# Kernel tuning notes

Hardware: AMD Instinct MI355X
Metric: run time of the kernel (lower is better)

The kernel has to match this reference:

```python
import jax, jax.numpy as jnp
import numpy as np

N_NODES = 10000
N_EDGES = 160000
IN_DIM, HID_DIM, OUT_DIM = 256, 512, 256


def gcn_conv(x, W, b, src, dst, dinv):
    # PyG GCNConv with add_self_loops=True and symmetric normalization.
    # dinv = deg^{-1/2} computed once (degrees include self loops).
    h = x @ W                                   # [N, F_out]
    norm = dinv[src] * dinv[dst]                # [E]
    msg = h[src] * norm[:, None]                # gather + scale, [E, F_out]
    agg = jnp.zeros_like(h).at[dst].add(msg)    # scatter-add over edges
    agg = agg + h * (dinv * dinv)[:, None]      # self-loop contribution
    return agg + b


def setup_inputs() -> dict:
    key = jax.random.key(0)
    ks = jax.random.split(key, 8)
    x = jax.random.normal(ks[0], (N_NODES, IN_DIM), dtype=jnp.float32)
    edge_index = jax.random.randint(ks[1], (2, N_EDGES), 0, N_NODES, dtype=jnp.int64)

    def glorot(k, fan_in, fan_out):
        s = jnp.sqrt(6.0 / (fan_in + fan_out)).astype(jnp.float32)
        return jax.random.uniform(k, (fan_in, fan_out), jnp.float32, -s, s)

    return {
        "x": x,
        "W1": glorot(ks[2], IN_DIM, HID_DIM), "b1": jnp.zeros((HID_DIM,), jnp.float32),
        "W2": glorot(ks[3], HID_DIM, HID_DIM), "b2": jnp.zeros((HID_DIM,), jnp.float32),
        "W3": glorot(ks[4], HID_DIM, OUT_DIM), "b3": jnp.zeros((OUT_DIM,), jnp.float32),
        "edge_index": edge_index,
    }


def reference(x, W1, b1, W2, b2, W3, b3, edge_index):
    src, dst = edge_index[0], edge_index[1]
    n = x.shape[0]
    # degree with self loops (edge weight 1), shared by all three layers
    deg = jnp.zeros((n,), x.dtype).at[dst].add(1.0) + 1.0
    dinv = jax.lax.rsqrt(deg)
    h = jnp.tanh(gcn_conv(x, W1, b1, src, dst, dinv))
    h = jnp.tanh(gcn_conv(h, W2, b2, src, dst, dinv))
    out = gcn_conv(h, W3, b3, src, dst, dinv)
    return out
```

## Files before the change

### kernel.cpp

```cpp
#include <hip/hip_runtime.h>
#include <math.h>

#define NN 10000
#define NE 160000
#define IN_DIM 256
#define HID_DIM 512
#define OUT_DIM 256

typedef unsigned short u16;
typedef _Float16 f16x8 __attribute__((ext_vector_type(8)));
typedef __attribute__((ext_vector_type(4))) float f32x4;


union F16U { _Float16 h; u16 u; };
static __device__ __forceinline__ u16 f2h_bits(float f) {
    F16U v; v.h = (_Float16)f; return v.u;
}

static __device__ __forceinline__ void gload_lds(const u16* g, uint4* l) {
    __builtin_amdgcn_global_load_lds((const __attribute__((address_space(1))) void*)g,
                                     (__attribute__((address_space(3))) void*)l,
                                     16, 0, 0);
}


__global__ void k_init(const float* __restrict__ W1, const float* __restrict__ W2,
                       const float* __restrict__ W3, const float* __restrict__ x,
                       u16* __restrict__ W1h, u16* __restrict__ W1l,
                       u16* __restrict__ W2h, u16* __restrict__ W2l,
                       u16* __restrict__ W3h, u16* __restrict__ W3l,
                       u16* __restrict__ xh, int* __restrict__ deg) {
    int idx = blockIdx.x * blockDim.x + threadIdx.x;
    const int S1 = IN_DIM * HID_DIM;
    const int S2 = HID_DIM * HID_DIM;
    const int S3 = HID_DIM * OUT_DIM;
    const int TW = S1 + S2 + S3;
    const int TX = NN * IN_DIM;
    if (idx < TW) {
        const float* W; u16 *Th, *Tl; int K, N, local;
        if (idx < S1)           { W = W1; Th = W1h; Tl = W1l; K = IN_DIM;  N = HID_DIM; local = idx; }
        else if (idx < S1 + S2) { W = W2; Th = W2h; Tl = W2l; K = HID_DIM; N = HID_DIM; local = idx - S1; }
        else                    { W = W3; Th = W3h; Tl = W3l; K = HID_DIM; N = OUT_DIM; local = idx - S1 - S2; }
        int k = local / N, n = local - k * N;
        float v = W[local];
        F16U hh; hh.h = (_Float16)v;
        float r = (v - (float)hh.h) * 2048.0f;
        Th[(size_t)n * K + k] = hh.u;
        Tl[(size_t)n * K + k] = f2h_bits(r);
    } else if (idx < TW + TX) {
        int j = idx - TW;
        xh[j] = f2h_bits(x[j]);
    } else if (idx < TW + TX + NN) {
        deg[idx - TW - TX] = 0;
    }
}


__global__ void k_count_deg(const int* __restrict__ dst, int* __restrict__ deg) {
    int e = blockIdx.x * blockDim.x + threadIdx.x;
    if (e < NE) atomicAdd(&deg[dst[e]], 1);
}

__launch_bounds__(1024)
__global__ void k_scan(const int* __restrict__ deg, int* __restrict__ row,
                       int* __restrict__ csr, float* __restrict__ dinv) {
    __shared__ int sdeg[10240];
    __shared__ int sums[1024];
    const int tid = threadIdx.x;
    for (int i = tid; i < NN; i += 1024) sdeg[i] = deg[i];
    __syncthreads();
    const int CH = 10;
    int base = tid * CH;
    int s = 0;
    for (int j = 0; j < CH; ++j) {
        int i = base + j;
        if (i < NN) s += sdeg[i] + 1;
    }
    sums[tid] = s;
    __syncthreads();
    for (int off = 1; off < 1024; off <<= 1) {
        int t = (tid >= off) ? sums[tid - off] : 0;
        __syncthreads();
        sums[tid] += t;
        __syncthreads();
    }
    int run = sums[tid] - s;
    for (int j = 0; j < CH; ++j) {
        int i = base + j;
        if (i < NN) {
            int dg = sdeg[i];
            csr[run] = i;
            row[i] = run + 1;
            dinv[i] = rsqrtf((float)dg + 1.0f);
            run += dg + 1;
        }
    }
}

__global__ void k_fill(const int* __restrict__ src, const int* __restrict__ dst,
                       int* __restrict__ row, int* __restrict__ csr) {
    int e = blockIdx.x * blockDim.x + threadIdx.x;
    if (e < NE) {
        int pos = atomicAdd(&row[dst[e]], 1);
        csr[pos] = src[e];
    }
}


template<int K, bool HAS_BIAS, bool DO_TANH, bool F16_OUT, bool ROWSCALE>
__launch_bounds__(256)
__global__ void k_gemm_f16x2(const u16* __restrict__ A, const u16* __restrict__ Bhi,
                             const u16* __restrict__ Blo,
                             const float* __restrict__ bias, const float* __restrict__ rowscale,
                             float* __restrict__ C, u16* __restrict__ Ch,
                             int M, int N, int MT, int MT8) {
    __shared__ uint4 As[2][512];
    __shared__ uint4 BsH[2][256];
    __shared__ uint4 BsL[2][256];

    const int id = blockIdx.x;
    const int xcd = id & 7;
    const int q2 = id >> 3;
    const int mt = (q2 % MT8) * 8 + xcd;
    const int nt = q2 / MT8;
    if (mt >= MT) return;

    const int tid  = threadIdx.x;
    const int wave = tid >> 6;
    const int lane = tid & 63;
    const int lr   = lane & 15;
    const int quad = lane >> 4;
    const int wm   = wave >> 1;
    const int wn   = wave & 1;
    const int m_base = mt * 128;
    const int n_base = nt * 64;

    const u16* gA  = A   + (size_t)(m_base + wave * 32 + lr) * K + quad * 8;
    const u16* gBh = Bhi + (size_t)(n_base + wave * 16 + lr) * K + quad * 8;
    const u16* gBl = Blo + (size_t)(n_base + wave * 16 + lr) * K + quad * 8;

    auto stage = [&](int buf, int it) {
        const int ko = it * 32;
        gload_lds(gA  + ko,          &As [buf][wave * 128]);
        gload_lds(gA  + ko + 16 * K, &As [buf][wave * 128 + 64]);
        gload_lds(gBh + ko,          &BsH[buf][wave * 64]);
        gload_lds(gBl + ko,          &BsL[buf][wave * 64]);
    };

    f32x4 accH[4][2] = {};
    f32x4 accL[4][2] = {};

    auto compute = [&](int buf) {
        f16x8 a[4], bH[2], bL[2];
#pragma unroll
        for (int tn = 0; tn < 2; ++tn) {
            int c = (wn * 2 + tn) * 64 + lane;
            bH[tn] = *(const f16x8*)&BsH[buf][c];
            bL[tn] = *(const f16x8*)&BsL[buf][c];
        }
#pragma unroll
        for (int tm = 0; tm < 4; ++tm)
            a[tm] = *(const f16x8*)&As[buf][(wm * 4 + tm) * 64 + lane];
#pragma unroll
        for (int tm = 0; tm < 4; ++tm)
#pragma unroll
            for (int tn = 0; tn < 2; ++tn) {
                accH[tm][tn] = __builtin_amdgcn_mfma_f32_16x16x32_f16(a[tm], bH[tn], accH[tm][tn], 0, 0, 0);
                accL[tm][tn] = __builtin_amdgcn_mfma_f32_16x16x32_f16(a[tm], bL[tn], accL[tm][tn], 0, 0, 0);
            }
    };

    const int NIT = K >> 5;

    stage(0, 0);
    __syncthreads();

    for (int it = 0; it < NIT; ++it) {
        if (it + 1 < NIT) stage((it + 1) & 1, it + 1);
        compute(it & 1);
        __syncthreads();
    }

#pragma unroll
    for (int tm = 0; tm < 4; ++tm) {
        int row0 = m_base + wm * 64 + tm * 16 + quad * 4;
#pragma unroll
        for (int i = 0; i < 4; ++i) {
            int row = row0 + i;
            if (row >= M) continue;
            float rs = ROWSCALE ? rowscale[row] : 1.0f;
#pragma unroll
            for (int tn = 0; tn < 2; ++tn) {
                int col = n_base + wn * 32 + tn * 16 + lr;
                float v = accH[tm][tn][i] + accL[tm][tn][i] * (1.0f / 2048.0f);
                if (HAS_BIAS) v += bias[col];
                if (DO_TANH) v = tanhf(v);
                if (ROWSCALE) v *= rs;
                if (F16_OUT) {
                    Ch[(size_t)row * N + col] = f2h_bits(v);
                } else {
                    C[(size_t)row * N + col] = v;
                }
            }
        }
    }
}


template<bool PRESCALED, bool HAS_BIAS, bool F16_OUT, int F>
__launch_bounds__(256)
__global__ void k_gather_h(const u16* __restrict__ h, const float* __restrict__ dinv,
                           const int* __restrict__ row_end, const int* __restrict__ csr,
                           const float* __restrict__ bias,
                           float* __restrict__ outF, u16* __restrict__ outH) {
    constexpr int L  = F / 8;
    constexpr int LS = L / 8;
    constexpr int NPB = 256 / LS;
    const int tid = threadIdx.x;
    const int d = (blockIdx.x >> 3) * NPB + tid / LS;
    if (d >= NN) return;
    const int f8 = (blockIdx.x & 7) * LS + (tid & (LS - 1));

    const int start = (d == 0) ? 0 : row_end[d - 1];
    const int end = row_end[d];
    const uint4* h16 = (const uint4*)h;

    float acc[8] = {};
    int e = start;
    for (; e + 8 <= end; e += 8) {
        int s[8]; uint4 raw[8]; float w[8];
#pragma unroll
        for (int j = 0; j < 8; ++j) s[j] = csr[e + j];
#pragma unroll
        for (int j = 0; j < 8; ++j) raw[j] = h16[(size_t)s[j] * L + f8];
#pragma unroll
        for (int j = 0; j < 8; ++j) w[j] = PRESCALED ? 1.0f : dinv[s[j]];
#pragma unroll
        for (int j = 0; j < 8; ++j) {
            f16x8 hv = *(const f16x8*)&raw[j];
#pragma unroll
            for (int t = 0; t < 8; ++t) acc[t] += w[j] * (float)hv[t];
        }
    }
    for (; e < end; ++e) {
        int s = csr[e];
        float w = PRESCALED ? 1.0f : dinv[s];
        uint4 raw = h16[(size_t)s * L + f8];
        f16x8 hv = *(const f16x8*)&raw;
#pragma unroll
        for (int t = 0; t < 8; ++t) acc[t] += w * (float)hv[t];
    }

    const float dd = dinv[d];
    float r[8];
#pragma unroll
    for (int t = 0; t < 8; ++t) r[t] = dd * acc[t];
    if (HAS_BIAS) {
        const float4* b4 = (const float4*)bias;
        float4 b0 = b4[f8 * 2], b1 = b4[f8 * 2 + 1];
        r[0] += b0.x; r[1] += b0.y; r[2] += b0.z; r[3] += b0.w;
        r[4] += b1.x; r[5] += b1.y; r[6] += b1.z; r[7] += b1.w;
    }
    if (F16_OUT) {
        union { u16 a[8]; uint4 v; } pk;
#pragma unroll
        for (int t = 0; t < 8; ++t) pk.a[t] = f2h_bits(r[t]);
        ((uint4*)outH)[(size_t)d * L + f8] = pk.v;
    } else {
        size_t base = (size_t)d * (F / 4) + f8 * 2;
        ((float4*)outF)[base]     = make_float4(r[0], r[1], r[2], r[3]);
        ((float4*)outF)[base + 1] = make_float4(r[4], r[5], r[6], r[7]);
    }
}


extern "C" void kernel_launch(void* const* d_in, const int* in_sizes, int n_in,
                              void* d_out, int out_size, void* d_ws, size_t ws_size,
                              hipStream_t stream) {
    const float* x  = (const float*)d_in[0];
    const float* W1 = (const float*)d_in[1];
    const float* b1 = (const float*)d_in[2];
    const float* W2 = (const float*)d_in[3];
    const float* b2 = (const float*)d_in[4];
    const float* W3 = (const float*)d_in[5];
    const float* b3 = (const float*)d_in[6];
    const int* edge = (const int*)d_in[7];
    const int* src = edge;
    const int* dst = edge + NE;
    float* out = (float*)d_out;

    const size_t SLOT = (size_t)NN * HID_DIM * 4;
    char* p = (char*)d_ws;
    char* slot0 = p;
    char* slot1 = p + SLOT;
    char* q = p + 2 * SLOT;
    u16* W1Th = (u16*)q; q += (size_t)IN_DIM  * HID_DIM * 2;
    u16* W1Tl = (u16*)q; q += (size_t)IN_DIM  * HID_DIM * 2;
    u16* W2Th = (u16*)q; q += (size_t)HID_DIM * HID_DIM * 2;
    u16* W2Tl = (u16*)q; q += (size_t)HID_DIM * HID_DIM * 2;
    u16* W3Th = (u16*)q; q += (size_t)HID_DIM * OUT_DIM * 2;
    u16* W3Tl = (u16*)q; q += (size_t)HID_DIM * OUT_DIM * 2;
    int*   deg  = (int*)q;   q += (size_t)NN * 4;
    float* dinv = (float*)q; q += (size_t)NN * 4;
    int*   row  = (int*)q;   q += (size_t)NN * 4;
    int*   csr  = (int*)q;   q += (size_t)(NE + NN) * 4;
    u16*   xh   = (u16*)q;   q += (size_t)NN * IN_DIM * 2;

    u16* Xagg  = (u16*)slot0;
    u16* g1h   = (u16*)slot1;
    u16* H1agg = (u16*)slot0;
    u16* h2    = (u16*)slot1;
    u16* g3h   = (u16*)slot0;

    const int T = 256;
    const int MT = (NN + 127) / 128;
    const int MT8 = (MT + 7) / 8;

    {
        int total = IN_DIM * HID_DIM + HID_DIM * HID_DIM + HID_DIM * OUT_DIM
                  + NN * IN_DIM + NN;
        k_init<<<(total + T - 1) / T, T, 0, stream>>>(W1, W2, W3, x, W1Th, W1Tl,
                                                      W2Th, W2Tl, W3Th, W3Tl, xh, deg);
    }
    k_count_deg<<<(NE + T - 1) / T, T, 0, stream>>>(dst, deg);
    k_scan<<<1, 1024, 0, stream>>>(deg, row, csr, dinv);
    k_fill<<<(NE + T - 1) / T, T, 0, stream>>>(src, dst, row, csr);

    const int G256 = ((NN + 63) / 64) * 8;
    const int G512 = ((NN + 31) / 32) * 8;
    const int GEMM_G512 = 8 * MT8 * (HID_DIM / 64);
    const int GEMM_G256 = 8 * MT8 * (OUT_DIM / 64);

    k_gather_h<false, false, true, IN_DIM><<<G256, 256, 0, stream>>>(
        xh, dinv, row, csr, nullptr, nullptr, Xagg);
    k_gemm_f16x2<IN_DIM, true, true, true, true><<<GEMM_G512, 256, 0, stream>>>(
        Xagg, W1Th, W1Tl, b1, dinv, nullptr, g1h, NN, HID_DIM, MT, MT8);

    k_gather_h<true, false, true, HID_DIM><<<G512, 256, 0, stream>>>(
        g1h, dinv, row, csr, nullptr, nullptr, H1agg);
    k_gemm_f16x2<HID_DIM, true, true, true, false><<<GEMM_G512, 256, 0, stream>>>(
        H1agg, W2Th, W2Tl, b2, nullptr, nullptr, h2, NN, HID_DIM, MT, MT8);

    k_gemm_f16x2<HID_DIM, false, false, true, true><<<GEMM_G256, 256, 0, stream>>>(
        h2, W3Th, W3Tl, nullptr, dinv, nullptr, g3h, NN, OUT_DIM, MT, MT8);
    k_gather_h<true, true, false, OUT_DIM><<<G256, 256, 0, stream>>>(
        g3h, dinv, row, csr, b3, out, nullptr);

    (void)in_sizes; (void)n_in; (void)out_size; (void)ws_size;
}
```

Measured before the change: 238.3 us.

## Fuse graph preprocessing kernels into one persistent kernel with grid barriers

Merges the init, degree count, scan and CSR fill kernels into a single persistent kernel of 512 blocks that uses atomic-counter grid barriers between phases, with a memset to zero the degree array and barrier counters. Weight and x conversion now runs after the CSR fill in the same kernel. The aim is to cut kernel launch overhead and the gaps between four small dependent launches. The risks are that a 512-block barrier needs every block co-resident to avoid deadlock, that the scan runs single-block while the other blocks spin, and that the grid-stride conversion loop serialises more work per thread.

Measured after the change: 671.0 us. +181.5%, slower.

```diff
diff --git a/kernel.cpp b/kernel.cpp
--- a/kernel.cpp
+++ b/kernel.cpp
@@ -7,6 +7,8 @@
 #define HID_DIM 512
 #define OUT_DIM 256
 
+#define PREP_GRID 512
+
 typedef unsigned short u16;
 typedef _Float16 f16x8 __attribute__((ext_vector_type(8)));
 typedef __attribute__((ext_vector_type(4))) float f32x4;
@@ -24,85 +26,93 @@
 }
 
 
-__global__ void k_init(const float* __restrict__ W1, const float* __restrict__ W2,
-                       const float* __restrict__ W3, const float* __restrict__ x,
-                       u16* __restrict__ W1h, u16* __restrict__ W1l,
-                       u16* __restrict__ W2h, u16* __restrict__ W2l,
-                       u16* __restrict__ W3h, u16* __restrict__ W3l,
-                       u16* __restrict__ xh, int* __restrict__ deg) {
-    int idx = blockIdx.x * blockDim.x + threadIdx.x;
+static __device__ __forceinline__ void gridbar(int* cnt) {
+    __syncthreads();
+    if (threadIdx.x == 0) {
+        __threadfence();
+        __hip_atomic_fetch_add(cnt, 1, __ATOMIC_ACQ_REL, __HIP_MEMORY_SCOPE_AGENT);
+        while (__hip_atomic_load(cnt, __ATOMIC_ACQUIRE, __HIP_MEMORY_SCOPE_AGENT) < PREP_GRID)
+            __builtin_amdgcn_s_sleep(1);
+    }
+    __syncthreads();
+}
+
+__global__ __launch_bounds__(256) void k_prep(
+    const float* __restrict__ W1, const float* __restrict__ W2,
+    const float* __restrict__ W3, const float* __restrict__ x,
+    const int* __restrict__ src, const int* __restrict__ dst,
+    u16* __restrict__ W1h, u16* __restrict__ W1l,
+    u16* __restrict__ W2h, u16* __restrict__ W2l,
+    u16* __restrict__ W3h, u16* __restrict__ W3l,
+    u16* __restrict__ xh, int* __restrict__ deg, int* __restrict__ row,
+    int* __restrict__ csr, float* __restrict__ dinv, int* __restrict__ bars) {
+    __shared__ int sdeg[10240];
+    __shared__ int psum[256];
+    const int tid = threadIdx.x;
+    const int gid = blockIdx.x * 256 + tid;
+    const int GS = PREP_GRID * 256;
+
+    for (int e = gid; e < NE; e += GS) atomicAdd(&deg[dst[e]], 1);
+    gridbar(&bars[0]);
+
+    if (blockIdx.x == 0) {
+        for (int i = tid; i < NN; i += 256)
+            sdeg[i] = __hip_atomic_load(&deg[i], __ATOMIC_RELAXED, __HIP_MEMORY_SCOPE_AGENT);
+        __syncthreads();
+        const int CH = 40;
+        const int base = tid * CH;
+        int s = 0;
+        for (int j = 0; j < CH; ++j) {
+            int i = base + j;
+            if (i < NN) s += sdeg[i] + 1;
+        }
+        psum[tid] = s;
+        __syncthreads();
+        for (int off = 1; off < 256; off <<= 1) {
+            int t = (tid >= off) ? psum[tid - off] : 0;
+            __syncthreads();
+            psum[tid] += t;
+            __syncthreads();
+        }
+        int run = psum[tid] - s;
+        for (int j = 0; j < CH; ++j) {
+            int i = base + j;
+            if (i < NN) {
+                int dg = sdeg[i];
+                csr[run] = i;
+                __hip_atomic_store(&row[i], run + 1, __ATOMIC_RELAXED, __HIP_MEMORY_SCOPE_AGENT);
+                dinv[i] = rsqrtf((float)dg + 1.0f);
+                run += dg + 1;
+            }
+        }
+    }
+    gridbar(&bars[1]);
+
+    for (int e = gid; e < NE; e += GS) {
+        int pos = atomicAdd(&row[dst[e]], 1);
+        csr[pos] = src[e];
+    }
     const int S1 = IN_DIM * HID_DIM;
     const int S2 = HID_DIM * HID_DIM;
     const int S3 = HID_DIM * OUT_DIM;
     const int TW = S1 + S2 + S3;
     const int TX = NN * IN_DIM;
-    if (idx < TW) {
-        const float* W; u16 *Th, *Tl; int K, N, local;
-        if (idx < S1)           { W = W1; Th = W1h; Tl = W1l; K = IN_DIM;  N = HID_DIM; local = idx; }
-        else if (idx < S1 + S2) { W = W2; Th = W2h; Tl = W2l; K = HID_DIM; N = HID_DIM; local = idx - S1; }
-        else                    { W = W3; Th = W3h; Tl = W3l; K = HID_DIM; N = OUT_DIM; local = idx - S1 - S2; }
-        int k = local / N, n = local - k * N;
-        float v = W[local];
-        F16U hh; hh.h = (_Float16)v;
-        float r = (v - (float)hh.h) * 2048.0f;
-        Th[(size_t)n * K + k] = hh.u;
-        Tl[(size_t)n * K + k] = f2h_bits(r);
-    } else if (idx < TW + TX) {
-        int j = idx - TW;
-        xh[j] = f2h_bits(x[j]);
-    } else if (idx < TW + TX + NN) {
-        deg[idx - TW - TX] = 0;
-    }
-}
-
-
-__global__ void k_count_deg(const int* __restrict__ dst, int* __restrict__ deg) {
-    int e = blockIdx.x * blockDim.x + threadIdx.x;
-    if (e < NE) atomicAdd(&deg[dst[e]], 1);
-}
-
-__launch_bounds__(1024)
-__global__ void k_scan(const int* __restrict__ deg, int* __restrict__ row,
-                       int* __restrict__ csr, float* __restrict__ dinv) {
-    __shared__ int sdeg[10240];
-    __shared__ int sums[1024];
-    const int tid = threadIdx.x;
-    for (int i = tid; i < NN; i += 1024) sdeg[i] = deg[i];
-    __syncthreads();
-    const int CH = 10;
-    int base = tid * CH;
-    int s = 0;
-    for (int j = 0; j < CH; ++j) {
-        int i = base + j;
-        if (i < NN) s += sdeg[i] + 1;
-    }
-    sums[tid] = s;
-    __syncthreads();
-    for (int off = 1; off < 1024; off <<= 1) {
-        int t = (tid >= off) ? sums[tid - off] : 0;
-        __syncthreads();
-        sums[tid] += t;
-        __syncthreads();
-    }
-    int run = sums[tid] - s;
-    for (int j = 0; j < CH; ++j) {
-        int i = base + j;
-        if (i < NN) {
-            int dg = sdeg[i];
-            csr[run] = i;
-            row[i] = run + 1;
-            dinv[i] = rsqrtf((float)dg + 1.0f);
-            run += dg + 1;
-        }
-    }
-}
-
-__global__ void k_fill(const int* __restrict__ src, const int* __restrict__ dst,
-                       int* __restrict__ row, int* __restrict__ csr) {
-    int e = blockIdx.x * blockDim.x + threadIdx.x;
-    if (e < NE) {
-        int pos = atomicAdd(&row[dst[e]], 1);
-        csr[pos] = src[e];
+    for (int idx = gid; idx < TW + TX; idx += GS) {
+        if (idx < TW) {
+            const float* W; u16 *Th, *Tl; int K, N, local;
+            if (idx < S1)           { W = W1; Th = W1h; Tl = W1l; K = IN_DIM;  N = HID_DIM; local = idx; }
+            else if (idx < S1 + S2) { W = W2; Th = W2h; Tl = W2l; K = HID_DIM; N = HID_DIM; local = idx - S1; }
+            else                    { W = W3; Th = W3h; Tl = W3l; K = HID_DIM; N = OUT_DIM; local = idx - S1 - S2; }
+            int k = local / N, n = local - k * N;
+            float v = W[local];
+            F16U hh; hh.h = (_Float16)v;
+            float r = (v - (float)hh.h) * 2048.0f;
+            Th[(size_t)n * K + k] = hh.u;
+            Tl[(size_t)n * K + k] = f2h_bits(r);
+        } else {
+            int j = idx - TW;
+            xh[j] = f2h_bits(x[j]);
+        }
     }
 }
 
@@ -301,6 +311,7 @@
     u16* W3Th = (u16*)q; q += (size_t)HID_DIM * OUT_DIM * 2;
     u16* W3Tl = (u16*)q; q += (size_t)HID_DIM * OUT_DIM * 2;
     int*   deg  = (int*)q;   q += (size_t)NN * 4;
+    int*   bars = (int*)q;   q += 16;
     float* dinv = (float*)q; q += (size_t)NN * 4;
     int*   row  = (int*)q;   q += (size_t)NN * 4;
     int*   csr  = (int*)q;   q += (size_t)(NE + NN) * 4;
@@ -312,19 +323,13 @@
     u16* h2    = (u16*)slot1;
     u16* g3h   = (u16*)slot0;
 
-    const int T = 256;
     const int MT = (NN + 127) / 128;
     const int MT8 = (MT + 7) / 8;
 
-    {
-        int total = IN_DIM * HID_DIM + HID_DIM * HID_DIM + HID_DIM * OUT_DIM
-                  + NN * IN_DIM + NN;
-        k_init<<<(total + T - 1) / T, T, 0, stream>>>(W1, W2, W3, x, W1Th, W1Tl,
-                                                      W2Th, W2Tl, W3Th, W3Tl, xh, deg);
-    }
-    k_count_deg<<<(NE + T - 1) / T, T, 0, stream>>>(dst, deg);
-    k_scan<<<1, 1024, 0, stream>>>(deg, row, csr, dinv);
-    k_fill<<<(NE + T - 1) / T, T, 0, stream>>>(src, dst, row, csr);
+    hipMemsetAsync(deg, 0, (size_t)NN * 4 + 16, stream);
+    k_prep<<<PREP_GRID, 256, 0, stream>>>(W1, W2, W3, x, src, dst,
+                                          W1Th, W1Tl, W2Th, W2Tl, W3Th, W3Tl,
+                                          xh, deg, row, csr, dinv, bars);
 
     const int G256 = ((NN + 63) / 64) * 8;
     const int G512 = ((NN + 31) / 32) * 8;
```
